# Kernel optimization log

Hardware: AMD Instinct MI355X
Metric: run time of the kernel (lower is better)

Reference implementation:

```python
import jax, jax.numpy as jnp
import numpy as np

VOCAB = 50257
EMB = 64
H = 32          # rnn_dim
SEQ = 256
BATCH = 16


def _gru_scan(x_seq, W_ih, W_hh, b_ih, b_hh):
    """Standard (PyTorch-convention) GRU over x_seq: (S, B, EMB) -> (S, B, H)."""
    gx = jnp.einsum('sbe,eh->sbh', x_seq, W_ih) + b_ih  # precompute input gates: (S,B,3H)
    h0 = jnp.zeros((x_seq.shape[1], H), dtype=x_seq.dtype)

    def step(h, gx_t):
        gh = h @ W_hh + b_hh                    # (B, 3H)
        xr, xz, xn = jnp.split(gx_t, 3, axis=-1)
        hr, hz, hn = jnp.split(gh, 3, axis=-1)
        r = jax.nn.sigmoid(xr + hr)
        z = jax.nn.sigmoid(xz + hz)
        n = jnp.tanh(xn + r * hn)
        h_new = (1.0 - z) * n + z * h
        return h_new, h_new

    _, hs = jax.lax.scan(step, h0, gx)
    return hs  # (S, B, H)


def setup_inputs() -> dict:
    key = jax.random.key(0)
    ks = jax.random.split(key, 13)
    s = 0.1  # keep random GRU weights in a stable range
    return {
        'input_batch': jax.random.randint(ks[0], (SEQ, BATCH), 0, VOCAB),
        'embed': jax.random.uniform(ks[1], (VOCAB, EMB), dtype=jnp.float32),
        'rnn_out': jax.random.uniform(ks[2], (2 * H, VOCAB), dtype=jnp.float32),
        'rnn_out_bias': jax.random.uniform(ks[3], (1, VOCAB), dtype=jnp.float32),
        'Wl_ih': jax.random.normal(ks[4], (EMB, 3 * H), dtype=jnp.float32) * s,
        'Wl_hh': jax.random.normal(ks[5], (H, 3 * H), dtype=jnp.float32) * s,
        'bl_ih': jax.random.normal(ks[6], (3 * H,), dtype=jnp.float32) * s,
        'bl_hh': jax.random.normal(ks[7], (3 * H,), dtype=jnp.float32) * s,
        'Wr_ih': jax.random.normal(ks[8], (EMB, 3 * H), dtype=jnp.float32) * s,
        'Wr_hh': jax.random.normal(ks[9], (H, 3 * H), dtype=jnp.float32) * s,
        'br_ih': jax.random.normal(ks[10], (3 * H,), dtype=jnp.float32) * s,
        'br_hh': jax.random.normal(ks[11], (3 * H,), dtype=jnp.float32) * s,
    }


def reference(input_batch, embed, rnn_out, rnn_out_bias,
              Wl_ih, Wl_hh, bl_ih, bl_hh,
              Wr_ih, Wr_hh, br_ih, br_hh):
    # Embedding lookup: (S, B, EMB)
    x = embed[input_batch]
    # Left-to-right GRU
    h_l = _gru_scan(x, Wl_ih, Wl_hh, bl_ih, bl_hh)
    # Right-to-left GRU: flip time, scan, flip back
    h_r = _gru_scan(x[::-1], Wr_ih, Wr_hh, br_ih, br_hh)[::-1]
    # Concat hidden states: (S, B, 2H)
    h = jnp.concatenate([h_l, h_r], axis=2)
    # Vocab projection + numerically stable log-softmax over dim=2
    logits = jnp.einsum('sbh,hv->sbv', h, rnn_out) + rnn_out_bias
    return jax.nn.log_softmax(logits, axis=2)
```

## Files before the change

### kernel.cpp

```cpp
#include <hip/hip_runtime.h>
#include <hip/hip_bf16.h>

#define SEQ 256
#define BATCH 16
#define MROWS 4096
#define EMB 64
#define HID 32
#define G3 96
#define KDIM 64
#define VOCAB 50257
#define VPAD 50304
#define NCHUNK (VPAD/128)

using short8 = __attribute__((ext_vector_type(8))) short;
using float4v = __attribute__((ext_vector_type(4))) float;

__device__ __forceinline__ short f2bf(float x) {
    unsigned u = __float_as_uint(x);
    u = (u + 0x7fffu + ((u >> 16) & 1u)) >> 16;
    return (short)u;
}

__global__ __launch_bounds__(128) void k_embed_gx(
    const int* __restrict__ idx, const float* __restrict__ embed,
    const float* __restrict__ Wl, const float* __restrict__ bl,
    const float* __restrict__ Wr, const float* __restrict__ br,
    float* __restrict__ gxl, float* __restrict__ gxr) {
  int row = blockIdx.x;
  int t = threadIdx.x;
  __shared__ float x[EMB];
  if (t < EMB) x[t] = embed[(size_t)idx[row] * EMB + t];
  __syncthreads();
  if (t < G3) {
    float al = bl[t], ar = br[t];
    #pragma unroll
    for (int e = 0; e < EMB; ++e) {
      float xe = x[e];
      al = fmaf(xe, Wl[e*G3 + t], al);
      ar = fmaf(xe, Wr[e*G3 + t], ar);
    }
    gxl[row*G3 + t] = al;
    gxr[row*G3 + t] = ar;
  }
}

__global__ __launch_bounds__(256) void k_transpose(
    const float* __restrict__ W, short* __restrict__ Wt) {
  __shared__ float tile[64][65];
  int v0 = blockIdx.x * 64;
  int t = threadIdx.x;
  #pragma unroll
  for (int i = 0; i < 16; ++i) {
    int e = i*256 + t;
    int k = e >> 6, v = e & 63;
    tile[k][v] = (v0 + v < VOCAB) ? W[(size_t)k*VOCAB + v0 + v] : 0.f;
  }
  __syncthreads();
  #pragma unroll
  for (int i = 0; i < 16; ++i) {
    int e = i*256 + t;
    int v = e >> 6, k = e & 63;
    Wt[(size_t)(v0 + v)*KDIM + k] = f2bf(tile[k][v]);
  }
}

__global__ __launch_bounds__(64) void k_gru(
    const float* __restrict__ gxl, const float* __restrict__ gxr,
    const float* __restrict__ Wlhh, const float* __restrict__ blhh,
    const float* __restrict__ Wrhh, const float* __restrict__ brhh,
    float* __restrict__ hbuf) {
  int chain = blockIdx.x;
  int dir = chain >> 4;
  int b = chain & 15;
  const float* gx  = dir ? gxr  : gxl;
  const float* Whh = dir ? Wrhh : Wlhh;
  const float* bhh = dir ? brhh : blhh;
  int l = threadIdx.x;
  int jA = l;
  int jB = 64 + (l & 31);
  float wA[HID], wB[HID];
  #pragma unroll
  for (int i = 0; i < HID; ++i) { wA[i] = Whh[i*G3 + jA]; wB[i] = Whh[i*G3 + jB]; }
  float bA = bhh[jA], bB = bhh[jB];
  __shared__ __align__(16) float hsh[HID];
  if (l < HID) hsh[l] = 0.f;
  int s0 = dir ? (SEQ-1) : 0;
  float gA = gx[(s0*BATCH + b)*G3 + jA];
  float gB = gx[(s0*BATCH + b)*G3 + jB];
  for (int t = 0; t < SEQ; ++t) {
    int s = dir ? (SEQ-1 - t) : t;
    int currow = s*BATCH + b;
    float gAn = 0.f, gBn = 0.f;
    if (t + 1 < SEQ) {
      int sn = dir ? (SEQ-2 - t) : (t+1);
      gAn = gx[(sn*BATCH + b)*G3 + jA];
      gBn = gx[(sn*BATCH + b)*G3 + jB];
    }
    float hv[HID];
    #pragma unroll
    for (int i = 0; i < 8; ++i) {
      float4v h4 = ((const float4v*)hsh)[i];
      hv[4*i+0]=h4[0]; hv[4*i+1]=h4[1]; hv[4*i+2]=h4[2]; hv[4*i+3]=h4[3];
    }
    float hold = hsh[l & 31];
    float accA = bA, accB = bB;
    #pragma unroll
    for (int i = 0; i < HID; ++i) {
      accA = fmaf(hv[i], wA[i], accA);
      accB = fmaf(hv[i], wB[i], accB);
    }
    float preA = gA + accA;
    float sig = 1.f / (1.f + __expf(-preA));
    float n = tanhf(gB + sig * accB);
    float z = __shfl(sig, 32 + (l & 31));
    float hnew = (1.f - z) * n + z * hold;
    if (l < HID) {
      hsh[l] = hnew;
      hbuf[currow*KDIM + dir*HID + l] = hnew;
    }
    gA = gAn; gB = gBn;
  }
}

__global__ __launch_bounds__(256) void k_lse(
    const float* __restrict__ hbuf, const short* __restrict__ Wt,
    const float* __restrict__ bias, float* __restrict__ rowsum) {
  int nb = blockIdx.x, mb = blockIdx.y, Nb = gridDim.x;
  int tid = threadIdx.x;
  int lane = tid & 63, wave = tid >> 6;
  int l15 = lane & 15, quad = lane >> 4;
  int m0 = mb*128 + wave*32;
  short8 afr[2][2];
  #pragma unroll
  for (int mt = 0; mt < 2; ++mt)
    #pragma unroll
    for (int kc = 0; kc < 2; ++kc) {
      const float* ap = hbuf + (m0 + mt*16 + l15)*KDIM + kc*32 + quad*8;
      float4v a0 = *(const float4v*)ap;
      float4v a1 = *(const float4v*)(ap + 4);
      short8 f;
      f[0]=f2bf(a0[0]); f[1]=f2bf(a0[1]); f[2]=f2bf(a0[2]); f[3]=f2bf(a0[3]);
      f[4]=f2bf(a1[0]); f[5]=f2bf(a1[1]); f[6]=f2bf(a1[2]); f[7]=f2bf(a1[3]);
      afr[mt][kc] = f;
    }
  float part[2][4] = {};
  for (int c = nb; c < NCHUNK; c += Nb) {
    int v0 = c*128;
    float4v acc[2][8];
    #pragma unroll
    for (int mt = 0; mt < 2; ++mt)
      #pragma unroll
      for (int nt = 0; nt < 8; ++nt)
        acc[mt][nt] = (float4v){0.f,0.f,0.f,0.f};
    #pragma unroll
    for (int kc = 0; kc < 2; ++kc)
      #pragma unroll
      for (int nt = 0; nt < 8; ++nt) {
        short8 bf = *(const short8*)(Wt + (size_t)(v0 + nt*16 + l15)*KDIM + kc*32 + quad*8);
        acc[0][nt] = __builtin_amdgcn_mfma_f32_16x16x32_bf16(afr[0][kc], bf, acc[0][nt], 0,0,0);
        acc[1][nt] = __builtin_amdgcn_mfma_f32_16x16x32_bf16(afr[1][kc], bf, acc[1][nt], 0,0,0);
      }
    #pragma unroll
    for (int nt = 0; nt < 8; ++nt) {
      int col = v0 + nt*16 + l15;
      bool ok = col < VOCAB;
      float bv = ok ? bias[col] : 0.f;
      #pragma unroll
      for (int mt = 0; mt < 2; ++mt)
        #pragma unroll
        for (int r = 0; r < 4; ++r) {
          float e = __expf(acc[mt][nt][r] + bv);
          part[mt][r] += ok ? e : 0.f;
        }
    }
  }
  #pragma unroll
  for (int mt = 0; mt < 2; ++mt)
    #pragma unroll
    for (int r = 0; r < 4; ++r) {
      float v = part[mt][r];
      v += __shfl_xor(v, 1);
      v += __shfl_xor(v, 2);
      v += __shfl_xor(v, 4);
      v += __shfl_xor(v, 8);
      if (l15 == 0) atomicAdd(&rowsum[m0 + mt*16 + quad*4 + r], v);
    }
}

__global__ __launch_bounds__(256) void k_out(
    const float* __restrict__ hbuf, const short* __restrict__ Wt,
    const float* __restrict__ bias, const float* __restrict__ rowsum,
    float* __restrict__ out) {
  int nb = blockIdx.x, mb = blockIdx.y, Nb = gridDim.x;
  int tid = threadIdx.x;
  int lane = tid & 63, wave = tid >> 6;
  int l15 = lane & 15, quad = lane >> 4;
  int m0 = mb*128 + wave*32;
  short8 afr[2][2];
  #pragma unroll
  for (int mt = 0; mt < 2; ++mt)
    #pragma unroll
    for (int kc = 0; kc < 2; ++kc) {
      const float* ap = hbuf + (m0 + mt*16 + l15)*KDIM + kc*32 + quad*8;
      float4v a0 = *(const float4v*)ap;
      float4v a1 = *(const float4v*)(ap + 4);
      short8 f;
      f[0]=f2bf(a0[0]); f[1]=f2bf(a0[1]); f[2]=f2bf(a0[2]); f[3]=f2bf(a0[3]);
      f[4]=f2bf(a1[0]); f[5]=f2bf(a1[1]); f[6]=f2bf(a1[2]); f[7]=f2bf(a1[3]);
      afr[mt][kc] = f;
    }
  float lse[2][4];
  #pragma unroll
  for (int mt = 0; mt < 2; ++mt)
    #pragma unroll
    for (int r = 0; r < 4; ++r)
      lse[mt][r] = logf(rowsum[m0 + mt*16 + quad*4 + r]);
  for (int c = nb; c < NCHUNK; c += Nb) {
    int v0 = c*128;
    float4v acc[2][8];
    #pragma unroll
    for (int mt = 0; mt < 2; ++mt)
      #pragma unroll
      for (int nt = 0; nt < 8; ++nt)
        acc[mt][nt] = (float4v){0.f,0.f,0.f,0.f};
    #pragma unroll
    for (int kc = 0; kc < 2; ++kc)
      #pragma unroll
      for (int nt = 0; nt < 8; ++nt) {
        short8 bf = *(const short8*)(Wt + (size_t)(v0 + nt*16 + l15)*KDIM + kc*32 + quad*8);
        acc[0][nt] = __builtin_amdgcn_mfma_f32_16x16x32_bf16(afr[0][kc], bf, acc[0][nt], 0,0,0);
        acc[1][nt] = __builtin_amdgcn_mfma_f32_16x16x32_bf16(afr[1][kc], bf, acc[1][nt], 0,0,0);
      }
    #pragma unroll
    for (int nt = 0; nt < 8; ++nt) {
      int col = v0 + nt*16 + l15;
      if (col < VOCAB) {
        float bv = bias[col];
        #pragma unroll
        for (int mt = 0; mt < 2; ++mt) {
          long base = (long)(m0 + mt*16 + quad*4) * VOCAB + col;
          #pragma unroll
          for (int r = 0; r < 4; ++r)
            out[base + (long)r*VOCAB] = acc[mt][nt][r] + bv - lse[mt][r];
        }
      }
    }
  }
}

extern "C" void kernel_launch(void* const* d_in, const int* in_sizes, int n_in,
                              void* d_out, int out_size, void* d_ws, size_t ws_size,
                              hipStream_t stream) {
  const int*   idx   = (const int*)d_in[0];
  const float* embed = (const float*)d_in[1];
  const float* W     = (const float*)d_in[2];
  const float* bias  = (const float*)d_in[3];
  const float* Wl_ih = (const float*)d_in[4];
  const float* Wl_hh = (const float*)d_in[5];
  const float* bl_ih = (const float*)d_in[6];
  const float* bl_hh = (const float*)d_in[7];
  const float* Wr_ih = (const float*)d_in[8];
  const float* Wr_hh = (const float*)d_in[9];
  const float* br_ih = (const float*)d_in[10];
  const float* br_hh = (const float*)d_in[11];
  float* out = (float*)d_out;
  char* ws = (char*)d_ws;
  float* gxl    = (float*)(ws);
  float* gxr    = (float*)(ws + 1572864);
  float* hbuf   = (float*)(ws + 3145728);
  float* rowsum = (float*)(ws + 4194304);
  short* Wt     = (short*)(ws + 4210688);

  hipMemsetAsync(rowsum, 0, MROWS*sizeof(float), stream);
  k_embed_gx<<<MROWS, 128, 0, stream>>>(idx, embed, Wl_ih, bl_ih, Wr_ih, br_ih, gxl, gxr);
  k_transpose<<<VPAD/64, 256, 0, stream>>>(W, Wt);
  k_gru<<<32, 64, 0, stream>>>(gxl, gxr, Wl_hh, bl_hh, Wr_hh, br_hh, hbuf);
  k_lse<<<dim3(32, 32), 256, 0, stream>>>(hbuf, Wt, bias, rowsum);
  k_out<<<dim3(64, 32), 256, 0, stream>>>(hbuf, Wt, bias, rowsum, out);
}
```

Before: 1.337 ms.

## Swap MFMA operands for row-contiguous output, merge prep kernels, speed GRU step

Swaps the A/B operands of the MFMA so each lane holds four consecutive vocab columns of one row. That lets k_out write 16-byte vector stores and k_lse load bias as a float4 from a padded bias buffer (-1e30 in padding) instead of masking each element. The embedding/gx and transpose kernels are merged into one launch, the GRU dot product is split into four independent accumulators with fast rcp/exp for sigmoid and tanh, and the k_lse grid is doubled. The faster transcendentals slightly change numerics, and the 16-byte stores are unaligned because VOCAB is odd.

New measurement: 1.270 ms. -5.0%, faster.

```diff
diff --git a/kernel.cpp b/kernel.cpp
--- a/kernel.cpp
+++ b/kernel.cpp
@@ -11,6 +11,7 @@
 #define VOCAB 50257
 #define VPAD 50304
 #define NCHUNK (VPAD/128)
+#define NTBLK (VPAD/64)
 
 using short8 = __attribute__((ext_vector_type(8))) short;
 using float4v = __attribute__((ext_vector_type(4))) float;
@@ -21,46 +22,57 @@
     return (short)u;
 }
 
-__global__ __launch_bounds__(128) void k_embed_gx(
+__device__ __forceinline__ void store16_u(float* p, float4v v) {
+    __builtin_memcpy((void*)p, &v, 16);
+}
+
+__global__ __launch_bounds__(256) void k_prep(
     const int* __restrict__ idx, const float* __restrict__ embed,
     const float* __restrict__ Wl, const float* __restrict__ bl,
     const float* __restrict__ Wr, const float* __restrict__ br,
-    float* __restrict__ gxl, float* __restrict__ gxr) {
-  int row = blockIdx.x;
+    float* __restrict__ gxl, float* __restrict__ gxr,
+    const float* __restrict__ W, short* __restrict__ Wt,
+    const float* __restrict__ bias, float* __restrict__ biasp) {
+  __shared__ float smem[64*65];
   int t = threadIdx.x;
-  __shared__ float x[EMB];
-  if (t < EMB) x[t] = embed[(size_t)idx[row] * EMB + t];
-  __syncthreads();
-  if (t < G3) {
-    float al = bl[t], ar = br[t];
-    #pragma unroll
-    for (int e = 0; e < EMB; ++e) {
-      float xe = x[e];
-      al = fmaf(xe, Wl[e*G3 + t], al);
-      ar = fmaf(xe, Wr[e*G3 + t], ar);
-    }
-    gxl[row*G3 + t] = al;
-    gxr[row*G3 + t] = ar;
-  }
-}
-
-__global__ __launch_bounds__(256) void k_transpose(
-    const float* __restrict__ W, short* __restrict__ Wt) {
-  __shared__ float tile[64][65];
-  int v0 = blockIdx.x * 64;
-  int t = threadIdx.x;
-  #pragma unroll
-  for (int i = 0; i < 16; ++i) {
-    int e = i*256 + t;
-    int k = e >> 6, v = e & 63;
-    tile[k][v] = (v0 + v < VOCAB) ? W[(size_t)k*VOCAB + v0 + v] : 0.f;
-  }
-  __syncthreads();
-  #pragma unroll
-  for (int i = 0; i < 16; ++i) {
-    int e = i*256 + t;
-    int v = e >> 6, k = e & 63;
-    Wt[(size_t)(v0 + v)*KDIM + k] = f2bf(tile[k][v]);
+  int blk = blockIdx.x;
+  if (blk < NTBLK) {
+    int v0 = blk * 64;
+    if (t < 64) {
+      int v = v0 + t;
+      biasp[v] = (v < VOCAB) ? bias[v] : -1e30f;
+    }
+    #pragma unroll
+    for (int i = 0; i < 16; ++i) {
+      int e = i*256 + t;
+      int k = e >> 6, v = e & 63;
+      smem[k*65 + v] = (v0 + v < VOCAB) ? W[(size_t)k*VOCAB + v0 + v] : 0.f;
+    }
+    __syncthreads();
+    #pragma unroll
+    for (int i = 0; i < 16; ++i) {
+      int e = i*256 + t;
+      int v = e >> 6, k = e & 63;
+      Wt[(size_t)(v0 + v)*KDIM + k] = f2bf(smem[k*65 + v]);
+    }
+  } else {
+    int row2 = blk - NTBLK;
+    int half = t >> 7, tt = t & 127;
+    int row = row2*2 + half;
+    float* x = smem + half*EMB;
+    if (tt < EMB) x[tt] = embed[(size_t)idx[row] * EMB + tt];
+    __syncthreads();
+    if (tt < G3) {
+      float al = bl[tt], ar = br[tt];
+      #pragma unroll
+      for (int e = 0; e < EMB; ++e) {
+        float xe = x[e];
+        al = fmaf(xe, Wl[e*G3 + tt], al);
+        ar = fmaf(xe, Wr[e*G3 + tt], ar);
+      }
+      gxl[row*G3 + tt] = al;
+      gxr[row*G3 + tt] = ar;
+    }
   }
 }
 
@@ -103,15 +115,26 @@
       hv[4*i+0]=h4[0]; hv[4*i+1]=h4[1]; hv[4*i+2]=h4[2]; hv[4*i+3]=h4[3];
     }
     float hold = hsh[l & 31];
-    float accA = bA, accB = bB;
-    #pragma unroll
-    for (int i = 0; i < HID; ++i) {
-      accA = fmaf(hv[i], wA[i], accA);
-      accB = fmaf(hv[i], wB[i], accB);
-    }
+    float aA0 = bA, aA1 = 0.f, aA2 = 0.f, aA3 = 0.f;
+    float aB0 = bB, aB1 = 0.f, aB2 = 0.f, aB3 = 0.f;
+    #pragma unroll
+    for (int i = 0; i < 8; ++i) {
+      aA0 = fmaf(hv[4*i+0], wA[4*i+0], aA0);
+      aA1 = fmaf(hv[4*i+1], wA[4*i+1], aA1);
+      aA2 = fmaf(hv[4*i+2], wA[4*i+2], aA2);
+      aA3 = fmaf(hv[4*i+3], wA[4*i+3], aA3);
+      aB0 = fmaf(hv[4*i+0], wB[4*i+0], aB0);
+      aB1 = fmaf(hv[4*i+1], wB[4*i+1], aB1);
+      aB2 = fmaf(hv[4*i+2], wB[4*i+2], aB2);
+      aB3 = fmaf(hv[4*i+3], wB[4*i+3], aB3);
+    }
+    float accA = (aA0 + aA1) + (aA2 + aA3);
+    float accB = (aB0 + aB1) + (aB2 + aB3);
     float preA = gA + accA;
-    float sig = 1.f / (1.f + __expf(-preA));
-    float n = tanhf(gB + sig * accB);
+    float sig = __builtin_amdgcn_rcpf(1.f + __expf(-preA));
+    float y = gB + sig * accB;
+    float e2 = __expf(2.f * y);
+    float n = 1.f - 2.f * __builtin_amdgcn_rcpf(e2 + 1.f);
     float z = __shfl(sig, 32 + (l & 31));
     float hnew = (1.f - z) * n + z * hold;
     if (l < HID) {
@@ -124,7 +147,7 @@
 
 __global__ __launch_bounds__(256) void k_lse(
     const float* __restrict__ hbuf, const short* __restrict__ Wt,
-    const float* __restrict__ bias, float* __restrict__ rowsum) {
+    const float* __restrict__ biasp, float* __restrict__ rowsum) {
   int nb = blockIdx.x, mb = blockIdx.y, Nb = gridDim.x;
   int tid = threadIdx.x;
   int lane = tid & 63, wave = tid >> 6;
@@ -143,7 +166,7 @@
       f[4]=f2bf(a1[0]); f[5]=f2bf(a1[1]); f[6]=f2bf(a1[2]); f[7]=f2bf(a1[3]);
       afr[mt][kc] = f;
     }
-  float part[2][4] = {};
+  float part[2] = {0.f, 0.f};
   for (int c = nb; c < NCHUNK; c += Nb) {
     int v0 = c*128;
     float4v acc[2][8];
@@ -156,40 +179,33 @@
     for (int kc = 0; kc < 2; ++kc)
       #pragma unroll
       for (int nt = 0; nt < 8; ++nt) {
-        short8 bf = *(const short8*)(Wt + (size_t)(v0 + nt*16 + l15)*KDIM + kc*32 + quad*8);
-        acc[0][nt] = __builtin_amdgcn_mfma_f32_16x16x32_bf16(afr[0][kc], bf, acc[0][nt], 0,0,0);
-        acc[1][nt] = __builtin_amdgcn_mfma_f32_16x16x32_bf16(afr[1][kc], bf, acc[1][nt], 0,0,0);
+        short8 wf = *(const short8*)(Wt + (size_t)(v0 + nt*16 + l15)*KDIM + kc*32 + quad*8);
+        acc[0][nt] = __builtin_amdgcn_mfma_f32_16x16x32_bf16(wf, afr[0][kc], acc[0][nt], 0,0,0);
+        acc[1][nt] = __builtin_amdgcn_mfma_f32_16x16x32_bf16(wf, afr[1][kc], acc[1][nt], 0,0,0);
       }
     #pragma unroll
     for (int nt = 0; nt < 8; ++nt) {
-      int col = v0 + nt*16 + l15;
-      bool ok = col < VOCAB;
-      float bv = ok ? bias[col] : 0.f;
+      int vb = v0 + nt*16 + quad*4;
+      float4v bv = *(const float4v*)(biasp + vb);
       #pragma unroll
       for (int mt = 0; mt < 2; ++mt)
         #pragma unroll
-        for (int r = 0; r < 4; ++r) {
-          float e = __expf(acc[mt][nt][r] + bv);
-          part[mt][r] += ok ? e : 0.f;
-        }
-    }
-  }
-  #pragma unroll
-  for (int mt = 0; mt < 2; ++mt)
-    #pragma unroll
-    for (int r = 0; r < 4; ++r) {
-      float v = part[mt][r];
-      v += __shfl_xor(v, 1);
-      v += __shfl_xor(v, 2);
-      v += __shfl_xor(v, 4);
-      v += __shfl_xor(v, 8);
-      if (l15 == 0) atomicAdd(&rowsum[m0 + mt*16 + quad*4 + r], v);
-    }
+        for (int r = 0; r < 4; ++r)
+          part[mt] += __expf(acc[mt][nt][r] + bv[r]);
+    }
+  }
+  #pragma unroll
+  for (int mt = 0; mt < 2; ++mt) {
+    float v = part[mt];
+    v += __shfl_xor(v, 16);
+    v += __shfl_xor(v, 32);
+    if (lane < 16) atomicAdd(&rowsum[m0 + mt*16 + l15], v);
+  }
 }
 
 __global__ __launch_bounds__(256) void k_out(
     const float* __restrict__ hbuf, const short* __restrict__ Wt,
-    const float* __restrict__ bias, const float* __restrict__ rowsum,
+    const float* __restrict__ biasp, const float* __restrict__ rowsum,
     float* __restrict__ out) {
   int nb = blockIdx.x, mb = blockIdx.y, Nb = gridDim.x;
   int tid = threadIdx.x;
@@ -209,12 +225,10 @@
       f[4]=f2bf(a1[0]); f[5]=f2bf(a1[1]); f[6]=f2bf(a1[2]); f[7]=f2bf(a1[3]);
       afr[mt][kc] = f;
     }
-  float lse[2][4];
+  float lsev[2];
   #pragma unroll
   for (int mt = 0; mt < 2; ++mt)
-    #pragma unroll
-    for (int r = 0; r < 4; ++r)
-      lse[mt][r] = logf(rowsum[m0 + mt*16 + quad*4 + r]);
+    lsev[mt] = __logf(rowsum[m0 + mt*16 + l15]);
   for (int c = nb; c < NCHUNK; c += Nb) {
     int v0 = c*128;
     float4v acc[2][8];
@@ -227,21 +241,36 @@
     for (int kc = 0; kc < 2; ++kc)
       #pragma unroll
       for (int nt = 0; nt < 8; ++nt) {
-        short8 bf = *(const short8*)(Wt + (size_t)(v0 + nt*16 + l15)*KDIM + kc*32 + quad*8);
-        acc[0][nt] = __builtin_amdgcn_mfma_f32_16x16x32_bf16(afr[0][kc], bf, acc[0][nt], 0,0,0);
-        acc[1][nt] = __builtin_amdgcn_mfma_f32_16x16x32_bf16(afr[1][kc], bf, acc[1][nt], 0,0,0);
-      }
-    #pragma unroll
-    for (int nt = 0; nt < 8; ++nt) {
-      int col = v0 + nt*16 + l15;
-      if (col < VOCAB) {
-        float bv = bias[col];
+        short8 wf = *(const short8*)(Wt + (size_t)(v0 + nt*16 + l15)*KDIM + kc*32 + quad*8);
+        acc[0][nt] = __builtin_amdgcn_mfma_f32_16x16x32_bf16(wf, afr[0][kc], acc[0][nt], 0,0,0);
+        acc[1][nt] = __builtin_amdgcn_mfma_f32_16x16x32_bf16(wf, afr[1][kc], acc[1][nt], 0,0,0);
+      }
+    if (v0 + 128 <= VOCAB) {
+      #pragma unroll
+      for (int nt = 0; nt < 8; ++nt) {
+        int vb = v0 + nt*16 + quad*4;
+        float4v bv = *(const float4v*)(biasp + vb);
         #pragma unroll
         for (int mt = 0; mt < 2; ++mt) {
-          long base = (long)(m0 + mt*16 + quad*4) * VOCAB + col;
+          long m = m0 + mt*16 + l15;
+          float4v o;
+          #pragma unroll
+          for (int r = 0; r < 4; ++r) o[r] = acc[mt][nt][r] + bv[r] - lsev[mt];
+          store16_u(out + m*VOCAB + vb, o);
+        }
+      }
+    } else {
+      #pragma unroll
+      for (int nt = 0; nt < 8; ++nt) {
+        int vb = v0 + nt*16 + quad*4;
+        float4v bv = *(const float4v*)(biasp + vb);
+        #pragma unroll
+        for (int mt = 0; mt < 2; ++mt) {
+          long m = m0 + mt*16 + l15;
           #pragma unroll
           for (int r = 0; r < 4; ++r)
-            out[base + (long)r*VOCAB] = acc[mt][nt][r] + bv - lse[mt][r];
+            if (vb + r < VOCAB)
+              out[m*VOCAB + vb + r] = acc[mt][nt][r] + bv[r] - lsev[mt];
         }
       }
     }
@@ -269,12 +298,13 @@
   float* gxr    = (float*)(ws + 1572864);
   float* hbuf   = (float*)(ws + 3145728);
   float* rowsum = (float*)(ws + 4194304);
-  short* Wt     = (short*)(ws + 4210688);
+  float* biasp  = (float*)(ws + 4210688);
+  short* Wt     = (short*)(ws + 4411904);
 
   hipMemsetAsync(rowsum, 0, MROWS*sizeof(float), stream);
-  k_embed_gx<<<MROWS, 128, 0, stream>>>(idx, embed, Wl_ih, bl_ih, Wr_ih, br_ih, gxl, gxr);
-  k_transpose<<<VPAD/64, 256, 0, stream>>>(W, Wt);
+  k_prep<<<NTBLK + 2048, 256, 0, stream>>>(idx, embed, Wl_ih, bl_ih, Wr_ih, br_ih,
+                                           gxl, gxr, W, Wt, bias, biasp);
   k_gru<<<32, 64, 0, stream>>>(gxl, gxr, Wl_hh, bl_hh, Wr_hh, br_hh, hbuf);
-  k_lse<<<dim3(32, 32), 256, 0, stream>>>(hbuf, Wt, bias, rowsum);
-  k_out<<<dim3(64, 32), 256, 0, stream>>>(hbuf, Wt, bias, rowsum, out);
-}
+  k_lse<<<dim3(64, 32), 256, 0, stream>>>(hbuf, Wt, biasp, rowsum);
+  k_out<<<dim3(64, 32), 256, 0, stream>>>(hbuf, Wt, biasp, rowsum, out);
+}
```
